# Performance work log

Measured on AMD Instinct MI355X. Metric: run time of the kernel, lower is better.

The kernel has to match this reference:

```python
import jax, jax.numpy as jnp
import numpy as np

B, I, H = 2048, 2048, 2048

def setup_inputs() -> dict:
    key = jax.random.key(0)
    ks = jax.random.split(key, 5)
    # Xavier-ish scale for weights
    W_ih = jax.random.normal(ks[0], (4 * H, I), jnp.float32) * (1.0 / np.sqrt(I))
    W_hh = jax.random.normal(ks[1], (4 * H, H), jnp.float32) * (1.0 / np.sqrt(H))
    b_ih = jnp.zeros((4 * H,), jnp.float32).at[H:2 * H].set(1.0)  # forget bias = 1
    b_hh = jnp.zeros((4 * H,), jnp.float32).at[H:2 * H].set(1.0)
    return {
        "x": jax.random.normal(ks[2], (B, I), jnp.float32),
        "h_prev": jax.random.normal(ks[3], (B, H), jnp.float32),
        "C_prev": jax.random.normal(ks[4], (B, H), jnp.float32),
        "W_ih": W_ih, "b_ih": b_ih, "W_hh": W_hh, "b_hh": b_hh,
    }

def reference(x, h_prev, C_prev, W_ih, b_ih, W_hh, b_hh):
    # Two GEMMs producing pre-activations for all four gates: [B, 4H]
    gates = jnp.dot(x, W_ih.T) + b_ih + jnp.dot(h_prev, W_hh.T) + b_hh
    gi, gf, gg, go = jnp.split(gates, 4, axis=1)  # torch chunk order: i, f, g, o
    input_gate = jax.nn.sigmoid(gi)
    forget_gate = jax.nn.sigmoid(gf)
    candidate_gate = jnp.tanh(gg)
    output_gate = jax.nn.sigmoid(go)
    new_C = forget_gate * C_prev + input_gate * candidate_gate
    new_h = output_gate * jnp.tanh(new_C)
    return (new_h, new_C, forget_gate, input_gate, candidate_gate, output_gate)
```

## Files before the change

### kernel.cpp

```cpp
#include <hip/hip_runtime.h>
#include <cstdint>
#include <cstddef>


typedef __attribute__((ext_vector_type(8))) short bf16x8;
typedef __attribute__((ext_vector_type(4))) float f32x4;

#define GLD_AS1 const __attribute__((address_space(1))) void
#define GLD_AS3 __attribute__((address_space(3))) void

__device__ __forceinline__ void gload_lds16(const void* g, void* l) {
  __builtin_amdgcn_global_load_lds((GLD_AS1*)g, (GLD_AS3*)l, 16, 0, 0);
}

__device__ __forceinline__ unsigned short f2bf(float f) {
  unsigned int u = __float_as_uint(f);
  unsigned int r = 0x7FFFu + ((u >> 16) & 1u);
  return (unsigned short)((u + r) >> 16);
}

__device__ __forceinline__ void barrier_f() {
  asm volatile("" ::: "memory");
  __builtin_amdgcn_s_barrier();
  asm volatile("" ::: "memory");
}

__global__ __launch_bounds__(256) void cvt_all(const float* __restrict__ x,
                                               const float* __restrict__ h,
                                               const float* __restrict__ Wih,
                                               const float* __restrict__ Whh,
                                               unsigned short* __restrict__ Abf,
                                               unsigned short* __restrict__ Wbf) {
  int bid = blockIdx.x;
  const float* src; unsigned short* dst; int col_off; int base;
  if (bid < 4096)        { src = x;   dst = Abf; col_off = 0;    base = bid; }
  else if (bid < 8192)   { src = h;   dst = Abf; col_off = 2048; base = bid - 4096; }
  else if (bid < 24576)  { src = Wih; dst = Wbf; col_off = 0;    base = bid - 8192; }
  else                   { src = Whh; dst = Wbf; col_off = 2048; base = bid - 24576; }
  int i = base * 256 + threadIdx.x;
  int flat = i << 2;
  int r = flat >> 11;
  int c = flat & 2047;
  float4 v = *(const float4*)(src + flat);
  ushort4 o;
  o.x = f2bf(v.x); o.y = f2bf(v.y); o.z = f2bf(v.z); o.w = f2bf(v.w);
  *(ushort4*)(dst + (((size_t)r) << 12) + col_off + c) = o;
}

__global__ __launch_bounds__(512, 2) void gemm_gates(
    const unsigned short* __restrict__ A,
    const unsigned short* __restrict__ W,
    const float* __restrict__ b_ih, const float* __restrict__ b_hh,
    float* __restrict__ gates)
{
  constexpr int N = 8192, K = 4096;
  constexpr int BK = 64;
  constexpr int NT = K / BK;
  __shared__ alignas(16) unsigned short lds[2][4][128 * 64];

  int b  = blockIdx.x;
  int xc = b & 7, ii = b >> 3;
  int bm = (ii & 7) * 256;
  int bn = (xc * 4 + (ii >> 3)) * 256;

  int tid  = threadIdx.x;
  int lane = tid & 63;
  int w    = tid >> 6;
  int wm   = w >> 2;
  int wn   = w & 3;
  int l15  = lane & 15;
  int lq   = lane >> 4;

  int ce0 = ((lq * 16) ^ ((l15 & 7) << 4)) >> 1;
  int ce1 = ((64 + lq * 16) ^ ((l15 & 7) << 4)) >> 1;

  int srow = 16 * w + (lane >> 3);
  int scol = ((lane & 7) ^ (lane >> 3)) * 8;
  const unsigned short* gA = A + (size_t)(bm + srow) * K + scol;
  const unsigned short* gB = W + (size_t)(bn + srow) * K + scol;

  f32x4 acc[8][4] = {};

  auto stageA = [&](int t, int h) {
    unsigned short* l0 = &lds[t & 1][h][w * 1024];
    const unsigned short* g = gA + (size_t)h * 128 * K + t * BK;
    gload_lds16(g, l0);
    gload_lds16(g + (size_t)8 * K, l0 + 512);
  };
  auto stageB = [&](int t, int h) {
    unsigned short* l0 = &lds[t & 1][2 + h][w * 1024];
    const unsigned short* g = gB + (size_t)h * 128 * K + t * BK;
    gload_lds16(g, l0);
    gload_lds16(g + (size_t)8 * K, l0 + 512);
  };

  stageA(0, 0); stageA(0, 1); stageB(0, 0); stageB(0, 1);
  stageB(1, 0); stageB(1, 1);

  bf16x8 af[4][2], bf01[2][2], bf23[2][2];

  for (int t = 0; t < NT; ++t) {
    if (t < NT - 1) asm volatile("s_waitcnt vmcnt(4)" ::: "memory");
    else            asm volatile("s_waitcnt vmcnt(0)" ::: "memory");
    barrier_f();

    const unsigned short* Ab = lds[t & 1][wm];
    const unsigned short* Bb = lds[t & 1][2 + (wn >> 1)];
    int brow = (wn & 1) * 64;

#pragma unroll
    for (int mt = 0; mt < 4; ++mt) {
      af[mt][0] = *(const bf16x8*)&Ab[(mt * 16 + l15) * 64 + ce0];
      af[mt][1] = *(const bf16x8*)&Ab[(mt * 16 + l15) * 64 + ce1];
    }
#pragma unroll
    for (int nt = 0; nt < 2; ++nt) {
      bf01[nt][0] = *(const bf16x8*)&Bb[(brow + nt * 16 + l15) * 64 + ce0];
      bf01[nt][1] = *(const bf16x8*)&Bb[(brow + nt * 16 + l15) * 64 + ce1];
    }
    if (t + 1 < NT) stageA(t + 1, 0);
    barrier_f();
    __builtin_amdgcn_s_setprio(1);
#pragma unroll
    for (int mt = 0; mt < 4; ++mt)
#pragma unroll
      for (int nt = 0; nt < 2; ++nt) {
        acc[mt][nt] = __builtin_amdgcn_mfma_f32_16x16x32_bf16(af[mt][0], bf01[nt][0], acc[mt][nt], 0, 0, 0);
        acc[mt][nt] = __builtin_amdgcn_mfma_f32_16x16x32_bf16(af[mt][1], bf01[nt][1], acc[mt][nt], 0, 0, 0);
      }
    __builtin_amdgcn_s_setprio(0);
    barrier_f();

#pragma unroll
    for (int nt = 0; nt < 2; ++nt) {
      bf23[nt][0] = *(const bf16x8*)&Bb[(brow + (2 + nt) * 16 + l15) * 64 + ce0];
      bf23[nt][1] = *(const bf16x8*)&Bb[(brow + (2 + nt) * 16 + l15) * 64 + ce1];
    }
    if (t + 1 < NT) stageA(t + 1, 1);
    barrier_f();
    __builtin_amdgcn_s_setprio(1);
#pragma unroll
    for (int mt = 0; mt < 4; ++mt)
#pragma unroll
      for (int nt = 0; nt < 2; ++nt) {
        acc[mt][2 + nt] = __builtin_amdgcn_mfma_f32_16x16x32_bf16(af[mt][0], bf23[nt][0], acc[mt][2 + nt], 0, 0, 0);
        acc[mt][2 + nt] = __builtin_amdgcn_mfma_f32_16x16x32_bf16(af[mt][1], bf23[nt][1], acc[mt][2 + nt], 0, 0, 0);
      }
    __builtin_amdgcn_s_setprio(0);
    barrier_f();

#pragma unroll
    for (int mt = 0; mt < 4; ++mt) {
      af[mt][0] = *(const bf16x8*)&Ab[(64 + mt * 16 + l15) * 64 + ce0];
      af[mt][1] = *(const bf16x8*)&Ab[(64 + mt * 16 + l15) * 64 + ce1];
    }
    if (t + 2 < NT) stageB(t + 2, 0);
    barrier_f();
    __builtin_amdgcn_s_setprio(1);
#pragma unroll
    for (int mt = 0; mt < 4; ++mt)
#pragma unroll
      for (int nt = 0; nt < 2; ++nt) {
        acc[4 + mt][2 + nt] = __builtin_amdgcn_mfma_f32_16x16x32_bf16(af[mt][0], bf23[nt][0], acc[4 + mt][2 + nt], 0, 0, 0);
        acc[4 + mt][2 + nt] = __builtin_amdgcn_mfma_f32_16x16x32_bf16(af[mt][1], bf23[nt][1], acc[4 + mt][2 + nt], 0, 0, 0);
      }
    __builtin_amdgcn_s_setprio(0);
    barrier_f();

    if (t + 2 < NT) stageB(t + 2, 1);
    barrier_f();
    __builtin_amdgcn_s_setprio(1);
#pragma unroll
    for (int mt = 0; mt < 4; ++mt)
#pragma unroll
      for (int nt = 0; nt < 2; ++nt) {
        acc[4 + mt][nt] = __builtin_amdgcn_mfma_f32_16x16x32_bf16(af[mt][0], bf01[nt][0], acc[4 + mt][nt], 0, 0, 0);
        acc[4 + mt][nt] = __builtin_amdgcn_mfma_f32_16x16x32_bf16(af[mt][1], bf01[nt][1], acc[4 + mt][nt], 0, 0, 0);
      }
    __builtin_amdgcn_s_setprio(0);
  }

#pragma unroll
  for (int nt = 0; nt < 4; ++nt) {
    int col = bn + wn * 64 + nt * 16 + l15;
    float bias = b_ih[col] + b_hh[col];
#pragma unroll
    for (int mt = 0; mt < 8; ++mt) {
      int row0 = bm + wm * 128 + mt * 16 + lq * 4;
#pragma unroll
      for (int j = 0; j < 4; ++j)
        gates[(size_t)(row0 + j) * N + col] = acc[mt][nt][j] + bias;
    }
  }
}

__device__ __forceinline__ float sigm(float x) { return 1.0f / (1.0f + __expf(-x)); }

__global__ __launch_bounds__(256) void lstm_epi(const float* __restrict__ gates,
                                                const float* __restrict__ C_prev,
                                                float* __restrict__ out, int total4) {
  int i = blockIdx.x * 256 + threadIdx.x;
  if (i >= total4) return;
  int flat = i << 2;
  int b = flat >> 11;
  int h = flat & 2047;
  const float* grow = gates + (((size_t)b) << 13);
  float4 vi = *(const float4*)(grow + h);
  float4 vf = *(const float4*)(grow + 2048 + h);
  float4 vg = *(const float4*)(grow + 4096 + h);
  float4 vo = *(const float4*)(grow + 6144 + h);
  float4 cp = *(const float4*)(C_prev + flat);

  float4 nh, nc, fg, ig, gg, og;
  const float* pi = (const float*)&vi;
  const float* pf = (const float*)&vf;
  const float* pg = (const float*)&vg;
  const float* po = (const float*)&vo;
  const float* pc = (const float*)&cp;
  float* onh = (float*)&nh; float* onc = (float*)&nc;
  float* ofg = (float*)&fg; float* oig = (float*)&ig;
  float* ogg = (float*)&gg; float* oog = (float*)&og;
#pragma unroll
  for (int j = 0; j < 4; ++j) {
    float I = sigm(pi[j]);
    float F = sigm(pf[j]);
    float G = tanhf(pg[j]);
    float O = sigm(po[j]);
    float C = F * pc[j] + I * G;
    float H = O * tanhf(C);
    oig[j] = I; ofg[j] = F; ogg[j] = G; oog[j] = O; onc[j] = C; onh[j] = H;
  }
  constexpr size_t SEC = (size_t)2048 * 2048;
  *(float4*)(out + 0 * SEC + flat) = nh;
  *(float4*)(out + 1 * SEC + flat) = nc;
  *(float4*)(out + 2 * SEC + flat) = fg;
  *(float4*)(out + 3 * SEC + flat) = ig;
  *(float4*)(out + 4 * SEC + flat) = gg;
  *(float4*)(out + 5 * SEC + flat) = og;
}

extern "C" void kernel_launch(void* const* d_in, const int* in_sizes, int n_in,
                              void* d_out, int out_size, void* d_ws, size_t ws_size,
                              hipStream_t stream) {
  const float* x   = (const float*)d_in[0];
  const float* h   = (const float*)d_in[1];
  const float* Cp  = (const float*)d_in[2];
  const float* Wih = (const float*)d_in[3];
  const float* bih = (const float*)d_in[4];
  const float* Whh = (const float*)d_in[5];
  const float* bhh = (const float*)d_in[6];
  float* out = (float*)d_out;

  uint8_t* ws = (uint8_t*)d_ws;
  unsigned short* Abf  = (unsigned short*)ws;
  unsigned short* Wbf  = (unsigned short*)(ws + (size_t)(16u << 20));
  float*          gates = (float*)(ws + (size_t)(80u << 20));

  cvt_all<<<40960, 256, 0, stream>>>(x, h, Wih, Whh, Abf, Wbf);
  gemm_gates<<<256, 512, 0, stream>>>(Abf, Wbf, bih, bhh, gates);
  lstm_epi<<<4096, 256, 0, stream>>>(gates, Cp, out, 1048576);
}
```

Before: 195.6 us.

## Fuse LSTM gate epilogue into GEMM by interleaving gate rows per tile

Each GEMM block now loads the i, f, g and o weight rows for the same 64 hidden units, so one tile holds all four gates for its hidden columns. The block applies the bias and the LSTM nonlinearities in registers and writes the six outputs directly. This removes the separate epilogue kernel and the fp32 gates round-trip through global memory (a 64 MB write plus read). In exchange, output stores are scalar and strided per lane rather than float4, and the GEMM tail takes on the transcendental work.

```diff
diff --git a/kernel.cpp b/kernel.cpp
--- a/kernel.cpp
+++ b/kernel.cpp
@@ -24,6 +24,8 @@
   __builtin_amdgcn_s_barrier();
   asm volatile("" ::: "memory");
 }
+
+__device__ __forceinline__ float sigm(float x) { return 1.0f / (1.0f + __expf(-x)); }
 
 __global__ __launch_bounds__(256) void cvt_all(const float* __restrict__ x,
                                                const float* __restrict__ h,
@@ -47,13 +49,14 @@
   *(ushort4*)(dst + (((size_t)r) << 12) + col_off + c) = o;
 }
 
-__global__ __launch_bounds__(512, 2) void gemm_gates(
+__global__ __launch_bounds__(512, 2) void gemm_lstm(
     const unsigned short* __restrict__ A,
     const unsigned short* __restrict__ W,
     const float* __restrict__ b_ih, const float* __restrict__ b_hh,
-    float* __restrict__ gates)
+    const float* __restrict__ C_prev,
+    float* __restrict__ out)
 {
-  constexpr int N = 8192, K = 4096;
+  constexpr int K = 4096;
   constexpr int BK = 64;
   constexpr int NT = K / BK;
   __shared__ alignas(16) unsigned short lds[2][4][128 * 64];
@@ -61,7 +64,7 @@
   int b  = blockIdx.x;
   int xc = b & 7, ii = b >> 3;
   int bm = (ii & 7) * 256;
-  int bn = (xc * 4 + (ii >> 3)) * 256;
+  int h0 = (xc * 4 + (ii >> 3)) * 64;
 
   int tid  = threadIdx.x;
   int lane = tid & 63;
@@ -74,22 +77,23 @@
   int ce0 = ((lq * 16) ^ ((l15 & 7) << 4)) >> 1;
   int ce1 = ((64 + lq * 16) ^ ((l15 & 7) << 4)) >> 1;
 
-  int srow = 16 * w + (lane >> 3);
+  int srow_s = lane >> 3;
   int scol = ((lane & 7) ^ (lane >> 3)) * 8;
-  const unsigned short* gA = A + (size_t)(bm + srow) * K + scol;
-  const unsigned short* gB = W + (size_t)(bn + srow) * K + scol;
+  const unsigned short* gA = A + (size_t)(bm + 16 * w + srow_s) * K + scol;
+  const unsigned short* gB0 =
+      W + (size_t)((w & 3) * 2048 + h0 + 16 * (w >> 2) + srow_s) * K + scol;
 
   f32x4 acc[8][4] = {};
 
-  auto stageA = [&](int t, int h) {
-    unsigned short* l0 = &lds[t & 1][h][w * 1024];
-    const unsigned short* g = gA + (size_t)h * 128 * K + t * BK;
+  auto stageA = [&](int t, int hh) {
+    unsigned short* l0 = &lds[t & 1][hh][w * 1024];
+    const unsigned short* g = gA + (size_t)hh * 128 * K + t * BK;
     gload_lds16(g, l0);
     gload_lds16(g + (size_t)8 * K, l0 + 512);
   };
-  auto stageB = [&](int t, int h) {
-    unsigned short* l0 = &lds[t & 1][2 + h][w * 1024];
-    const unsigned short* g = gB + (size_t)h * 128 * K + t * BK;
+  auto stageB = [&](int t, int hh) {
+    unsigned short* l0 = &lds[t & 1][2 + hh][w * 1024];
+    const unsigned short* g = gB0 + (size_t)hh * 32 * K + t * BK;
     gload_lds16(g, l0);
     gload_lds16(g + (size_t)8 * K, l0 + 512);
   };
@@ -180,63 +184,32 @@
     __builtin_amdgcn_s_setprio(0);
   }
 
-#pragma unroll
-  for (int nt = 0; nt < 4; ++nt) {
-    int col = bn + wn * 64 + nt * 16 + l15;
-    float bias = b_ih[col] + b_hh[col];
-#pragma unroll
-    for (int mt = 0; mt < 8; ++mt) {
-      int row0 = bm + wm * 128 + mt * 16 + lq * 4;
-#pragma unroll
-      for (int j = 0; j < 4; ++j)
-        gates[(size_t)(row0 + j) * N + col] = acc[mt][nt][j] + bias;
+  int hcol = h0 + wn * 16 + l15;
+  float cb0 = b_ih[hcol]          + b_hh[hcol];
+  float cb1 = b_ih[2048 + hcol]   + b_hh[2048 + hcol];
+  float cb2 = b_ih[4096 + hcol]   + b_hh[4096 + hcol];
+  float cb3 = b_ih[6144 + hcol]   + b_hh[6144 + hcol];
+  constexpr size_t SEC = (size_t)2048 * 2048;
+#pragma unroll
+  for (int mt = 0; mt < 8; ++mt) {
+    int row0 = bm + wm * 128 + mt * 16 + lq * 4;
+#pragma unroll
+    for (int j = 0; j < 4; ++j) {
+      size_t off = (size_t)(row0 + j) * 2048 + hcol;
+      float I = sigm(acc[mt][0][j] + cb0);
+      float F = sigm(acc[mt][1][j] + cb1);
+      float G = tanhf(acc[mt][2][j] + cb2);
+      float O = sigm(acc[mt][3][j] + cb3);
+      float C = F * C_prev[off] + I * G;
+      float H = O * tanhf(C);
+      out[0 * SEC + off] = H;
+      out[1 * SEC + off] = C;
+      out[2 * SEC + off] = F;
+      out[3 * SEC + off] = I;
+      out[4 * SEC + off] = G;
+      out[5 * SEC + off] = O;
     }
   }
-}
-
-__device__ __forceinline__ float sigm(float x) { return 1.0f / (1.0f + __expf(-x)); }
-
-__global__ __launch_bounds__(256) void lstm_epi(const float* __restrict__ gates,
-                                                const float* __restrict__ C_prev,
-                                                float* __restrict__ out, int total4) {
-  int i = blockIdx.x * 256 + threadIdx.x;
-  if (i >= total4) return;
-  int flat = i << 2;
-  int b = flat >> 11;
-  int h = flat & 2047;
-  const float* grow = gates + (((size_t)b) << 13);
-  float4 vi = *(const float4*)(grow + h);
-  float4 vf = *(const float4*)(grow + 2048 + h);
-  float4 vg = *(const float4*)(grow + 4096 + h);
-  float4 vo = *(const float4*)(grow + 6144 + h);
-  float4 cp = *(const float4*)(C_prev + flat);
-
-  float4 nh, nc, fg, ig, gg, og;
-  const float* pi = (const float*)&vi;
-  const float* pf = (const float*)&vf;
-  const float* pg = (const float*)&vg;
-  const float* po = (const float*)&vo;
-  const float* pc = (const float*)&cp;
-  float* onh = (float*)&nh; float* onc = (float*)&nc;
-  float* ofg = (float*)&fg; float* oig = (float*)&ig;
-  float* ogg = (float*)&gg; float* oog = (float*)&og;
-#pragma unroll
-  for (int j = 0; j < 4; ++j) {
-    float I = sigm(pi[j]);
-    float F = sigm(pf[j]);
-    float G = tanhf(pg[j]);
-    float O = sigm(po[j]);
-    float C = F * pc[j] + I * G;
-    float H = O * tanhf(C);
-    oig[j] = I; ofg[j] = F; ogg[j] = G; oog[j] = O; onc[j] = C; onh[j] = H;
-  }
-  constexpr size_t SEC = (size_t)2048 * 2048;
-  *(float4*)(out + 0 * SEC + flat) = nh;
-  *(float4*)(out + 1 * SEC + flat) = nc;
-  *(float4*)(out + 2 * SEC + flat) = fg;
-  *(float4*)(out + 3 * SEC + flat) = ig;
-  *(float4*)(out + 4 * SEC + flat) = gg;
-  *(float4*)(out + 5 * SEC + flat) = og;
 }
 
 extern "C" void kernel_launch(void* const* d_in, const int* in_sizes, int n_in,
@@ -254,9 +227,7 @@
   uint8_t* ws = (uint8_t*)d_ws;
   unsigned short* Abf  = (unsigned short*)ws;
   unsigned short* Wbf  = (unsigned short*)(ws + (size_t)(16u << 20));
-  float*          gates = (float*)(ws + (size_t)(80u << 20));
 
   cvt_all<<<40960, 256, 0, stream>>>(x, h, Wih, Whh, Abf, Wbf);
-  gemm_gates<<<256, 512, 0, stream>>>(Abf, Wbf, bih, bhh, gates);
-  lstm_epi<<<4096, 256, 0, stream>>>(gates, Cp, out, 1048576);
-}
+  gemm_lstm<<<256, 512, 0, stream>>>(Abf, Wbf, bih, bhh, Cp, out);
+}
```

New measurement: 186.6 us. -4.6%, faster.
